# Kernel optimization log

Hardware: AMD Instinct MI355X
Metric: run time of the kernel (lower is better)

Reference implementation:

```python
import jax, jax.numpy as jnp
import numpy as np
from jax import lax

NPOINT = 1024
RADIUS = 0.2
NSAMPLE = 32


def fps(xyz, npoint):
    """Furthest point sampling on one cloud. xyz: (N,3) -> (npoint,) int32."""
    n = xyz.shape[0]
    init_d = jnp.full((n,), 1e10, xyz.dtype)

    def body(carry, _):
        dists, last_idx = carry
        last = xyz[last_idx]
        d = jnp.sum((xyz - last) ** 2, axis=-1)
        dists = jnp.minimum(dists, d)
        nxt = jnp.argmax(dists).astype(jnp.int32)
        return (dists, nxt), nxt

    (_, _), idxs = lax.scan(body, (init_d, jnp.int32(0)), None, length=npoint - 1)
    return jnp.concatenate([jnp.zeros((1,), jnp.int32), idxs])


def ball_query(xyz, new_xyz, radius, nsample):
    """First `nsample` points of xyz within `radius` of each center (pad with first hit).
    xyz: (N,3), new_xyz: (S,3) -> (S,nsample) int32."""
    n = xyz.shape[0]
    d2 = jnp.sum((new_xyz[:, None, :] - xyz[None, :, :]) ** 2, axis=-1)  # (S,N)
    cand = jnp.where(d2 < radius * radius, jnp.arange(n, dtype=jnp.int32)[None, :], n)
    idx = jnp.sort(cand, axis=1)[:, :nsample]                            # (S,K)
    first = jnp.where(idx[:, :1] == n, 0, idx[:, :1])
    return jnp.where(idx == n, first, idx)


def setup_inputs() -> dict:
    key = jax.random.key(0)
    ks = jax.random.split(key, 8)
    C_in = 64 + 3  # features + relative xyz
    W1 = jax.random.normal(ks[0], (64, C_in), jnp.float32) * (1.0 / np.sqrt(C_in))
    b1 = jnp.zeros((64,), jnp.float32)
    W2 = jax.random.normal(ks[1], (128, 64), jnp.float32) * (1.0 / np.sqrt(64))
    b2 = jnp.zeros((128,), jnp.float32)
    W3 = jax.random.normal(ks[2], (256, 128), jnp.float32) * (1.0 / np.sqrt(128))
    b3 = jnp.zeros((256,), jnp.float32)
    xyz = jax.random.uniform(ks[3], (8, 4096, 3), jnp.float32)
    features = jax.random.normal(ks[4], (8, 4096, 64), jnp.float32)
    return {"xyz": xyz, "features": features, "W1": W1, "b1": b1,
            "W2": W2, "b2": b2, "W3": W3, "b3": b3}


def reference(xyz, features, W1, b1, W2, b2, W3, b3):
    def per_batch(xyz_b, feat_b):
        fps_idx = fps(xyz_b, NPOINT)                      # (S,)
        new_xyz = xyz_b[fps_idx]                          # (S,3)
        idx = ball_query(xyz_b, new_xyz, RADIUS, NSAMPLE)  # (S,K)
        g_xyz = xyz_b[idx] - new_xyz[:, None, :]          # (S,K,3) relative coords
        g_feat = feat_b[idx]                              # (S,K,C)
        g = jnp.concatenate([g_xyz, g_feat], axis=-1)     # (S,K,3+C)
        x = jnp.transpose(g, (2, 0, 1))                   # (C',S,K)
        for W, b in ((W1, b1), (W2, b2), (W3, b3)):       # 1x1 conv + ReLU stack
            x = jax.nn.relu(jnp.einsum('oc,csk->osk', W, x) + b[:, None, None])
        return new_xyz, jnp.max(x, axis=-1), fps_idx      # max-pool over nsample

    new_xyz, new_features, sample_inds = jax.vmap(per_batch)(xyz, features)
    return new_xyz, new_features, sample_inds
```

## Files before the change

kernel.cpp:

```cpp
#include <hip/hip_runtime.h>
#include <stdint.h>

#define N_PTS 4096
#define S_PTS 1024
#define K_SAMP 32

typedef __attribute__((ext_vector_type(8))) short bf16x8;
typedef __attribute__((ext_vector_type(4))) float f32x4;

#define GT1_S 104
#define GT2_S 72
#define GT3_S 136

__device__ __forceinline__ short f2b(float f){
  unsigned u = __float_as_uint(f);
  u = u + 0x7fffu + ((u >> 16) & 1u);
  return (short)(u >> 16);
}

#define DPP_QUAD_XOR1 0xB1
#define DPP_QUAD_XOR2 0x4E
#define DPP_ROW_HMIRR 0x141
#define DPP_ROW_MIRR  0x140
#define DPP_ROW_BC15  0x142
#define DPP_ROW_BC31  0x143

template<int CTRL>
__device__ __forceinline__ unsigned long long kstep(unsigned long long k){
  unsigned lo = (unsigned)k, hi = (unsigned)(k >> 32);
  unsigned lo2 = (unsigned)__builtin_amdgcn_update_dpp((int)lo, (int)lo, CTRL, 0xF, 0xF, false);
  unsigned hi2 = (unsigned)__builtin_amdgcn_update_dpp((int)hi, (int)hi, CTRL, 0xF, 0xF, false);
  unsigned long long ok = ((unsigned long long)hi2 << 32) | lo2;
  return ok > k ? ok : k;
}

__global__ __launch_bounds__(256) void fps_kernel(const float* __restrict__ xyz,
                                                  float* __restrict__ out_newxyz,
                                                  float* __restrict__ out_inds){
  __shared__ float4 c4[N_PTS];
  __shared__ unsigned long long slots[2][4];
  const int b = blockIdx.x;
  const int t = threadIdx.x;
  const int lane = t & 63;
  const int w = t >> 6;
  const float* xb = xyz + (size_t)b * N_PTS * 3;

  float px[16], py[16], pz[16], dist[16];
#pragma unroll
  for (int j = 0; j < 16; ++j){
    int p = j * 256 + t;
    float x = xb[p*3+0], y = xb[p*3+1], z = xb[p*3+2];
    px[j] = x; py[j] = y; pz[j] = z; dist[j] = 1e10f;
    c4[p] = make_float4(x, y, z, 0.0f);
  }
  __syncthreads();

  float lx, ly, lz;
  { float4 c0 = c4[0]; lx = c0.x; ly = c0.y; lz = c0.z; }
  if (t == 0){
    out_inds[(size_t)b * S_PTS] = 0.0f;
    out_newxyz[(size_t)b*S_PTS*3 + 0] = lx;
    out_newxyz[(size_t)b*S_PTS*3 + 1] = ly;
    out_newxyz[(size_t)b*S_PTS*3 + 2] = lz;
  }

  for (int it = 1; it < S_PTS; ++it){
    float bv = -1.0f; int bj = 0;
#pragma unroll
    for (int j = 0; j < 16; ++j){
      float dx = __fsub_rn(px[j], lx);
      float dy = __fsub_rn(py[j], ly);
      float dz = __fsub_rn(pz[j], lz);
      float d  = __fadd_rn(__fadd_rn(__fmul_rn(dx,dx), __fmul_rn(dy,dy)), __fmul_rn(dz,dz));
      float nd = fminf(dist[j], d);
      dist[j] = nd;
      bool gt = nd > bv;
      bv = gt ? nd : bv;
      bj = gt ? j  : bj;
    }
    int bi = bj * 256 + t;
    unsigned long long k = ((unsigned long long)__float_as_uint(bv) << 32)
                         | (unsigned)(~bi);

    k = kstep<DPP_QUAD_XOR1>(k);
    k = kstep<DPP_QUAD_XOR2>(k);
    k = kstep<DPP_ROW_HMIRR>(k);
    k = kstep<DPP_ROW_MIRR >(k);
    k = kstep<DPP_ROW_BC15 >(k);
    k = kstep<DPP_ROW_BC31 >(k);

    if (lane == 63) slots[it & 1][w] = k;
    __syncthreads();

    unsigned long long sk = slots[it & 1][lane & 3];
    sk = kstep<DPP_QUAD_XOR1>(sk);
    sk = kstep<DPP_QUAD_XOR2>(sk);
    int cur = (int)(~(unsigned)sk);

    float4 cc = c4[cur];
    lx = cc.x; ly = cc.y; lz = cc.z;
    if (t == 0){
      out_inds[(size_t)b*S_PTS + it] = (float)cur;
      out_newxyz[((size_t)b*S_PTS + it)*3 + 0] = lx;
      out_newxyz[((size_t)b*S_PTS + it)*3 + 1] = ly;
      out_newxyz[((size_t)b*S_PTS + it)*3 + 2] = lz;
    }
  }
}

__global__ void wconv_kernel(const float* __restrict__ W1,
                             const float* __restrict__ W2,
                             const float* __restrict__ W3,
                             short* __restrict__ ws_w){
  short* w1 = ws_w;
  short* w2 = ws_w + 64*96;
  short* w3 = ws_w + 64*96 + 128*64;
  int t = blockIdx.x * blockDim.x + threadIdx.x;
  int stride = gridDim.x * blockDim.x;
  for (int i = t; i < 64*96; i += stride){
    int m = i / 96, k = i - m*96;
    float v = 0.0f;
    if (k < 64)      v = W1[m*67 + 3 + k];
    else if (k < 67) v = W1[m*67 + (k - 64)];
    w1[i] = f2b(v);
  }
  for (int i = t; i < 128*64;  i += stride) w2[i] = f2b(W2[i]);
  for (int i = t; i < 256*128; i += stride) w3[i] = f2b(W3[i]);
}

__global__ __launch_bounds__(256) void ballquery_kernel(const float* __restrict__ xyz,
                                                        const float* __restrict__ newxyz,
                                                        int* __restrict__ idx_ws){
  const int lane = threadIdx.x & 63;
  const int c = blockIdx.x * 4 + (threadIdx.x >> 6);
  const int b = c >> 10;
  const float* xb = xyz + (size_t)b * N_PTS * 3;
  const float cx = newxyz[(size_t)c*3+0];
  const float cy = newxyz[(size_t)c*3+1];
  const float cz = newxyz[(size_t)c*3+2];
  const float R2 = 0.2f * 0.2f;
  int* idxp = idx_ws + (size_t)c * K_SAMP;
  int have = 0, first = -1;
  for (int chunk = 0; chunk < 64 && have < K_SAMP; ++chunk){
    int p = chunk * 64 + lane;
    float dx = __fsub_rn(xb[p*3+0], cx);
    float dy = __fsub_rn(xb[p*3+1], cy);
    float dz = __fsub_rn(xb[p*3+2], cz);
    float d2 = __fadd_rn(__fadd_rn(__fmul_rn(dx,dx), __fmul_rn(dy,dy)), __fmul_rn(dz,dz));
    bool hit = d2 < R2;
    unsigned long long mask = __ballot(hit);
    if (mask){
      if (first < 0) first = chunk*64 + (__ffsll(mask) - 1);
      int pre = __popcll(mask & ((1ull << lane) - 1ull));
      if (hit && (have + pre) < K_SAMP) idxp[have + pre] = p;
      have += __popcll(mask);
      if (have > K_SAMP) have = K_SAMP;
    }
  }
  if (first < 0) first = 0;
  if (lane < K_SAMP - have) idxp[have + lane] = first;
}

template<int M, int KC, int KPAD, int GS_IN, int GS_OUT>
__device__ __forceinline__ void layer_mfma(const short* __restrict__ Wl,
                                           const short* gin, short* gout,
                                           const float* __restrict__ sbias_l,
                                           int w, int quad, int col){
  for (int m0 = w*16; m0 < M; m0 += 64){
    f32x4 acc0 = {0,0,0,0}, acc1 = {0,0,0,0};
#pragma unroll
    for (int kc = 0; kc < KC; ++kc){
      bf16x8 a  = *reinterpret_cast<const bf16x8*>(Wl + (size_t)(m0+col)*KPAD + kc*32 + quad*8);
      bf16x8 b0 = *reinterpret_cast<const bf16x8*>(gin + col*GS_IN + kc*32 + quad*8);
      bf16x8 b1 = *reinterpret_cast<const bf16x8*>(gin + (16+col)*GS_IN + kc*32 + quad*8);
      acc0 = __builtin_amdgcn_mfma_f32_16x16x32_bf16(a, b0, acc0, 0, 0, 0);
      acc1 = __builtin_amdgcn_mfma_f32_16x16x32_bf16(a, b1, acc1, 0, 0, 0);
    }
    int rbase = m0 + quad*4;
    unsigned long long P0 = 0ull, P1 = 0ull;
#pragma unroll
    for (int r = 0; r < 4; ++r){
      float bias = sbias_l[rbase + r];
      unsigned long long q0 = (unsigned short)f2b(fmaxf(acc0[r] + bias, 0.0f));
      unsigned long long q1 = (unsigned short)f2b(fmaxf(acc1[r] + bias, 0.0f));
      P0 |= q0 << (16*r);
      P1 |= q1 << (16*r);
    }
    *reinterpret_cast<unsigned long long*>(&gout[col*GS_OUT + rbase])      = P0;
    *reinterpret_cast<unsigned long long*>(&gout[(16+col)*GS_OUT + rbase]) = P1;
  }
}

__global__ __launch_bounds__(256) void mlp_kernel(const float* __restrict__ xyz,
                                                  const float* __restrict__ feat,
                                                  const float* __restrict__ b1,
                                                  const float* __restrict__ b2,
                                                  const float* __restrict__ b3,
                                                  const float* __restrict__ newxyz,
                                                  const int* __restrict__ idx_ws,
                                                  const short* __restrict__ ws_w,
                                                  float* __restrict__ pooled){
  __shared__ __align__(16) short gT1[32*GT1_S];
  __shared__ __align__(16) short gT2[32*GT2_S];
  __shared__ __align__(16) short gT3[32*GT3_S];
  __shared__ int   sidx[32];
  __shared__ float sbias[448];
  const int t = threadIdx.x;
  const int c = blockIdx.x;
  const int b = c >> 10;
  const int lane = t & 63;
  const int w = t >> 6;
  const int quad = lane >> 4;
  const int col = lane & 15;

  const short* w1 = ws_w;
  const short* w2 = ws_w + 64*96;
  const short* w3 = ws_w + 64*96 + 128*64;

  if (t < 32) sidx[t] = idx_ws[(size_t)c*K_SAMP + t];
  for (int i = t; i < 448; i += 256)
    sbias[i] = (i < 64) ? b1[i] : (i < 192) ? b2[i-64] : b3[i-192];
  for (int i = t; i < 32*GT1_S; i += 256) gT1[i] = 0;
  __syncthreads();

  {
    int p = t >> 3, q = t & 7;
    int src = sidx[p];
    const float* fr = feat + ((size_t)b * N_PTS + src) * 64 + q*8;
    unsigned u[4];
#pragma unroll
    for (int jj = 0; jj < 4; ++jj){
      unsigned lo = (unsigned short)f2b(fr[2*jj]);
      unsigned hi = (unsigned short)f2b(fr[2*jj+1]);
      u[jj] = lo | (hi << 16);
    }
    uint4 v; v.x = u[0]; v.y = u[1]; v.z = u[2]; v.w = u[3];
    *reinterpret_cast<uint4*>(&gT1[p*GT1_S + q*8]) = v;
  }
  if (t < 32){
    int src = sidx[t];
    const float* pr = xyz + ((size_t)b * N_PTS + src) * 3;
    float cx = newxyz[(size_t)c*3+0];
    float cy = newxyz[(size_t)c*3+1];
    float cz = newxyz[(size_t)c*3+2];
    gT1[t*GT1_S + 64] = f2b(__fsub_rn(pr[0], cx));
    gT1[t*GT1_S + 65] = f2b(__fsub_rn(pr[1], cy));
    gT1[t*GT1_S + 66] = f2b(__fsub_rn(pr[2], cz));
  }
  __syncthreads();

  layer_mfma<64, 3, 96, GT1_S, GT2_S>(w1, gT1, gT2, sbias, w, quad, col);
  __syncthreads();
  layer_mfma<128, 2, 64, GT2_S, GT3_S>(w2, gT2, gT3, sbias + 64, w, quad, col);
  __syncthreads();

  for (int m0 = w*16; m0 < 256; m0 += 64){
    f32x4 acc0 = {0,0,0,0}, acc1 = {0,0,0,0};
#pragma unroll
    for (int kc = 0; kc < 4; ++kc){
      bf16x8 a  = *reinterpret_cast<const bf16x8*>(w3 + (size_t)(m0+col)*128 + kc*32 + quad*8);
      bf16x8 b0 = *reinterpret_cast<const bf16x8*>(gT3 + col*GT3_S + kc*32 + quad*8);
      bf16x8 b1 = *reinterpret_cast<const bf16x8*>(gT3 + (16+col)*GT3_S + kc*32 + quad*8);
      acc0 = __builtin_amdgcn_mfma_f32_16x16x32_bf16(a, b0, acc0, 0, 0, 0);
      acc1 = __builtin_amdgcn_mfma_f32_16x16x32_bf16(a, b1, acc1, 0, 0, 0);
    }
    float vm[4];
#pragma unroll
    for (int r = 0; r < 4; ++r) vm[r] = fmaxf(acc0[r], acc1[r]);
#pragma unroll
    for (int off = 1; off < 16; off <<= 1){
#pragma unroll
      for (int r = 0; r < 4; ++r) vm[r] = fmaxf(vm[r], __shfl_xor(vm[r], off, 16));
    }
    if (col == 0){
#pragma unroll
      for (int r = 0; r < 4; ++r){
        int ch = m0 + quad*4 + r;
        pooled[(size_t)c*256 + ch] = fmaxf(vm[r] + sbias[192 + ch], 0.0f);
      }
    }
  }
}

__global__ __launch_bounds__(256) void transpose_kernel(const float* __restrict__ pooled,
                                                        float* __restrict__ outf){
  __shared__ float tile[64][65];
  int b  = blockIdx.z;
  int s0 = blockIdx.x * 64;
  int c0 = blockIdx.y * 64;
#pragma unroll
  for (int k = 0; k < 16; ++k){
    int idx = threadIdx.x + k*256;
    int si = idx >> 6, ci = idx & 63;
    tile[si][ci] = pooled[((size_t)b*S_PTS + s0 + si)*256 + c0 + ci];
  }
  __syncthreads();
#pragma unroll
  for (int k = 0; k < 16; ++k){
    int idx = threadIdx.x + k*256;
    int ci = idx >> 6, si = idx & 63;
    outf[((size_t)b*256 + c0 + ci)*S_PTS + s0 + si] = tile[si][ci];
  }
}

extern "C" void kernel_launch(void* const* d_in, const int* in_sizes, int n_in,
                              void* d_out, int out_size, void* d_ws, size_t ws_size,
                              hipStream_t stream){
  const float* xyz  = (const float*)d_in[0];
  const float* feat = (const float*)d_in[1];
  const float* W1   = (const float*)d_in[2];
  const float* b1   = (const float*)d_in[3];
  const float* W2   = (const float*)d_in[4];
  const float* b2   = (const float*)d_in[5];
  const float* W3   = (const float*)d_in[6];
  const float* b3   = (const float*)d_in[7];

  float* out        = (float*)d_out;
  float* out_newxyz = out;
  float* out_feat   = out + 24576;
  float* out_inds   = out + 24576 + 2097152;

  char*  ws     = (char*)d_ws;
  short* ws_w   = (short*)ws;
  int*   idx_ws = (int*)(ws + 94208);
  float* pooled = (float*)(ws + 94208 + 1048576);

  wconv_kernel<<<32, 256, 0, stream>>>(W1, W2, W3, ws_w);
  fps_kernel<<<8, 256, 0, stream>>>(xyz, out_newxyz, out_inds);
  ballquery_kernel<<<2048, 256, 0, stream>>>(xyz, out_newxyz, idx_ws);
  mlp_kernel<<<8192, 256, 0, stream>>>(xyz, feat, b1, b2, b3, out_newxyz,
                                       idx_ws, ws_w, pooled);
  transpose_kernel<<<dim3(16, 4, 8), 256, 0, stream>>>(pooled, out_feat);
}
```

Measured before the change: 797.3 us.

## Restructure FPS argmax into packed distance math and two-phase float/index wave reduction

The furthest-point-sampling loop now computes distances with two-wide float vectors to allow packed FP32 instructions. The per-lane argmax becomes a tree max followed by an equality-based index search. The cross-lane reduction uses a 32-bit float DPP max plus ballot/readlane for the index, with a fallback DPP min on ties, instead of a 64-bit key reduction. The final cross-wave step reads all four slots and takes a scalar max rather than doing a DPP reduction. This aims to shorten the serial 1023-iteration critical path, at the cost of extra compares and a possible divergent tie branch.

```diff
diff --git a/kernel.cpp b/kernel.cpp
--- a/kernel.cpp
+++ b/kernel.cpp
@@ -7,6 +7,7 @@
 
 typedef __attribute__((ext_vector_type(8))) short bf16x8;
 typedef __attribute__((ext_vector_type(4))) float f32x4;
+typedef __attribute__((ext_vector_type(2))) float f32x2;
 
 #define GT1_S 104
 #define GT2_S 72
@@ -26,31 +27,41 @@
 #define DPP_ROW_BC31  0x143
 
 template<int CTRL>
-__device__ __forceinline__ unsigned long long kstep(unsigned long long k){
-  unsigned lo = (unsigned)k, hi = (unsigned)(k >> 32);
-  unsigned lo2 = (unsigned)__builtin_amdgcn_update_dpp((int)lo, (int)lo, CTRL, 0xF, 0xF, false);
-  unsigned hi2 = (unsigned)__builtin_amdgcn_update_dpp((int)hi, (int)hi, CTRL, 0xF, 0xF, false);
-  unsigned long long ok = ((unsigned long long)hi2 << 32) | lo2;
-  return ok > k ? ok : k;
+__device__ __forceinline__ float fstep(float v){
+  int o = __builtin_amdgcn_update_dpp(__float_as_int(v), __float_as_int(v),
+                                      CTRL, 0xF, 0xF, false);
+  return fmaxf(v, __int_as_float(o));
+}
+template<int CTRL>
+__device__ __forceinline__ unsigned ustep(unsigned v){
+  unsigned o = (unsigned)__builtin_amdgcn_update_dpp((int)v, (int)v,
+                                                     CTRL, 0xF, 0xF, false);
+  return o < v ? o : v;
+}
+__device__ __forceinline__ unsigned long long umax64(unsigned long long a,
+                                                     unsigned long long b){
+  return a > b ? a : b;
 }
 
 __global__ __launch_bounds__(256) void fps_kernel(const float* __restrict__ xyz,
                                                   float* __restrict__ out_newxyz,
                                                   float* __restrict__ out_inds){
+#pragma clang fp contract(off)
   __shared__ float4 c4[N_PTS];
-  __shared__ unsigned long long slots[2][4];
+  __shared__ __align__(16) unsigned long long slots[2][4];
   const int b = blockIdx.x;
   const int t = threadIdx.x;
   const int lane = t & 63;
   const int w = t >> 6;
   const float* xb = xyz + (size_t)b * N_PTS * 3;
 
-  float px[16], py[16], pz[16], dist[16];
+  f32x2 px2[8], py2[8], pz2[8], dist2[8];
 #pragma unroll
   for (int j = 0; j < 16; ++j){
     int p = j * 256 + t;
     float x = xb[p*3+0], y = xb[p*3+1], z = xb[p*3+2];
-    px[j] = x; py[j] = y; pz[j] = z; dist[j] = 1e10f;
+    px2[j>>1][j&1] = x; py2[j>>1][j&1] = y; pz2[j>>1][j&1] = z;
+    dist2[j>>1][j&1] = 1e10f;
     c4[p] = make_float4(x, y, z, 0.0f);
   }
   __syncthreads();
@@ -65,37 +76,72 @@
   }
 
   for (int it = 1; it < S_PTS; ++it){
-    float bv = -1.0f; int bj = 0;
-#pragma unroll
-    for (int j = 0; j < 16; ++j){
-      float dx = __fsub_rn(px[j], lx);
-      float dy = __fsub_rn(py[j], ly);
-      float dz = __fsub_rn(pz[j], lz);
-      float d  = __fadd_rn(__fadd_rn(__fmul_rn(dx,dx), __fmul_rn(dy,dy)), __fmul_rn(dz,dz));
-      float nd = fminf(dist[j], d);
-      dist[j] = nd;
-      bool gt = nd > bv;
-      bv = gt ? nd : bv;
-      bj = gt ? j  : bj;
-    }
-    int bi = bj * 256 + t;
-    unsigned long long k = ((unsigned long long)__float_as_uint(bv) << 32)
-                         | (unsigned)(~bi);
-
-    k = kstep<DPP_QUAD_XOR1>(k);
-    k = kstep<DPP_QUAD_XOR2>(k);
-    k = kstep<DPP_ROW_HMIRR>(k);
-    k = kstep<DPP_ROW_MIRR >(k);
-    k = kstep<DPP_ROW_BC15 >(k);
-    k = kstep<DPP_ROW_BC31 >(k);
-
-    if (lane == 63) slots[it & 1][w] = k;
+    f32x2 vlx = {lx, lx}, vly = {ly, ly}, vlz = {lz, lz};
+    float bq[8];
+#pragma unroll
+    for (int q = 0; q < 8; ++q){
+      f32x2 dx = px2[q] - vlx;
+      f32x2 dy = py2[q] - vly;
+      f32x2 dz = pz2[q] - vlz;
+      f32x2 m1 = dx * dx;
+      f32x2 m2 = dy * dy;
+      f32x2 m3 = dz * dz;
+      f32x2 s  = (m1 + m2) + m3;
+      f32x2 nd;
+      nd[0] = fminf(dist2[q][0], s[0]);
+      nd[1] = fminf(dist2[q][1], s[1]);
+      dist2[q] = nd;
+      bq[q] = fmaxf(nd[0], nd[1]);
+    }
+#pragma unroll
+    for (int s = 4; s >= 1; s >>= 1)
+#pragma unroll
+      for (int q = 0; q < s; ++q) bq[q] = fmaxf(bq[q], bq[q+s]);
+    float bv = bq[0];
+
+    int idxs[16];
+#pragma unroll
+    for (int j = 0; j < 16; ++j)
+      idxs[j] = (dist2[j>>1][j&1] == bv) ? j : 1024;
+#pragma unroll
+    for (int s = 8; s >= 1; s >>= 1)
+#pragma unroll
+      for (int j = 0; j < s; ++j) idxs[j] = min(idxs[j], idxs[j+s]);
+    int bi = (idxs[0] << 8) + t;
+
+    float wm = bv;
+    wm = fstep<DPP_QUAD_XOR1>(wm);
+    wm = fstep<DPP_QUAD_XOR2>(wm);
+    wm = fstep<DPP_ROW_HMIRR>(wm);
+    wm = fstep<DPP_ROW_MIRR >(wm);
+    wm = fstep<DPP_ROW_BC15 >(wm);
+    wm = fstep<DPP_ROW_BC31 >(wm);
+    float smax = __int_as_float(__builtin_amdgcn_readlane(__float_as_int(wm), 63));
+
+    unsigned long long m = __ballot(bv == smax);
+    int wbi;
+    if (__popcll(m) == 1){
+      wbi = __builtin_amdgcn_readlane(bi, (int)(__ffsll(m) - 1));
+    } else {
+      unsigned mi = (bv == smax) ? (unsigned)bi : 0xFFFFFFFFu;
+      mi = ustep<DPP_QUAD_XOR1>(mi);
+      mi = ustep<DPP_QUAD_XOR2>(mi);
+      mi = ustep<DPP_ROW_HMIRR>(mi);
+      mi = ustep<DPP_ROW_MIRR >(mi);
+      mi = ustep<DPP_ROW_BC15 >(mi);
+      mi = ustep<DPP_ROW_BC31 >(mi);
+      wbi = (int)__builtin_amdgcn_readlane(mi, 63);
+    }
+
+    if (lane == 0)
+      slots[it & 1][w] = (((unsigned long long)__float_as_uint(smax)) << 32)
+                       | (unsigned)(~wbi);
     __syncthreads();
 
-    unsigned long long sk = slots[it & 1][lane & 3];
-    sk = kstep<DPP_QUAD_XOR1>(sk);
-    sk = kstep<DPP_QUAD_XOR2>(sk);
-    int cur = (int)(~(unsigned)sk);
+    const unsigned long long* sp = slots[it & 1];
+    unsigned long long k0 = sp[0], k1 = sp[1], k2 = sp[2], k3 = sp[3];
+    unsigned long long kk = umax64(umax64(k0, k1), umax64(k2, k3));
+    int cur = (int)(~(unsigned)kk);
 
     float4 cc = c4[cur];
     lx = cc.x; ly = cc.y; lz = cc.z;
```

Measured after the change: 808.8 us. No clear change (+1.4%).
